# Kernel tuning notes

Measured on AMD Instinct MI355X. Metric: run time of the kernel, lower is better.

Reference implementation:

```python
import jax, jax.numpy as jnp
import numpy as np

B, T, D, H = 2, 4096, 512, 8
DH = D // H  # dim_head = 64


def setup_inputs() -> dict:
    key = jax.random.key(0)
    ks = jax.random.split(key, 10)
    s = 1.0 / np.sqrt(D)
    x = jax.random.normal(ks[0], (B, T, D), dtype=jnp.float32)
    Wq = jax.random.uniform(ks[1], (D, D), jnp.float32, -s, s)
    Wk = jax.random.uniform(ks[2], (D, D), jnp.float32, -s, s)
    Wv = jax.random.uniform(ks[3], (D, D), jnp.float32, -s, s)
    Wo = jax.random.uniform(ks[4], (D, D), jnp.float32, -s, s)
    bq = jnp.zeros((D,), jnp.float32)
    bk = jnp.zeros((D,), jnp.float32)
    bv = jnp.zeros((D,), jnp.float32)
    bo = jnp.zeros((D,), jnp.float32)
    mask = jax.random.randint(ks[5], (1, 1, T, T), 0, 2).astype(bool)
    return {"x": x, "Wq": Wq, "bq": bq, "Wk": Wk, "bk": bk,
            "Wv": Wv, "bv": bv, "Wo": Wo, "bo": bo, "mask": mask}


def reference(x, Wq, bq, Wk, bk, Wv, bv, Wo, bo, mask):
    # QKV projections (self-attention: Q=K=V=x)
    def split_heads(t):
        return t.reshape(B, T, H, DH).transpose(0, 2, 1, 3)  # (B,H,T,DH)
    Q = split_heads(x @ Wq + bq)
    K = split_heads(x @ Wk + bk)
    V = split_heads(x @ Wv + bv)
    # scaled dot-product attention with additive mask penalty (as in source)
    scores = jnp.einsum('bhqd,bhkd->bhqk', Q, K) / np.sqrt(DH)
    scores = scores + (~mask).astype(scores.dtype) * (-1e9)
    att_w = jax.nn.softmax(scores, axis=-1)
    O = jnp.einsum('bhqk,bhkd->bhqd', att_w, V)
    O = O.transpose(0, 2, 1, 3).reshape(B, T, D)
    return O @ Wo + bo
```

## Files before the change

kernel.cpp:

```cpp
#include <hip/hip_runtime.h>
#include <stdint.h>

#define B_ 2
#define T_ 4096
#define D_ 512
#define H_ 8
#define DH_ 64

typedef __bf16 bf16;
typedef __bf16 bf16x4_t __attribute__((ext_vector_type(4)));
typedef __bf16 bf16x8_t __attribute__((ext_vector_type(8)));
typedef float f32x4 __attribute__((ext_vector_type(4)));
typedef short short4_t __attribute__((ext_vector_type(4)));
typedef uint32_t u32;

static constexpr float QSCALE = 0.18033688011112042f;

__device__ __forceinline__ void async16(void* lds, const void* g) {
  __builtin_amdgcn_global_load_lds(
      (const __attribute__((address_space(1))) void*)g,
      (__attribute__((address_space(3))) void*)lds, 16, 0, 0);
}

__global__ __launch_bounds__(256) void prep_kernel(
    const float* __restrict__ x,
    const float* __restrict__ Wq, const float* __restrict__ Wk,
    const float* __restrict__ Wv, const float* __restrict__ Wo,
    const void* __restrict__ maskp,
    bf16* __restrict__ xb, bf16* __restrict__ WTall, bf16* __restrict__ WoT,
    u32* __restrict__ bmask)
{
  int bid = blockIdx.x;
  int tid = threadIdx.x;
  if (bid < 4096) {
    int idx = bid * 256 + tid;
    const float4* xf = (const float4*)x;
    float4 v = xf[idx];
    bf16x4_t o;
    o[0] = (bf16)v.x; o[1] = (bf16)v.y; o[2] = (bf16)v.z; o[3] = (bf16)v.w;
    ((bf16x4_t*)xb)[idx] = o;
  } else if (bid < 8192) {
    int gid = (bid - 4096) * 256 + tid;
    int sel = gid >> 18;
    int idx = gid & 262143;
    int n = idx >> 9, k = idx & 511;
    if (sel < 3) {
      const float* W = (sel == 0) ? Wq : (sel == 1) ? Wk : Wv;
      float v = W[k * 512 + n];
      if (sel == 0) v *= QSCALE;
      WTall[gid] = (bf16)v;
    } else {
      WoT[idx] = (bf16)Wo[k * 512 + n];
    }
  } else {
    int wid = (bid - 8192) * 256 + tid;
    const uint8_t* m8 = (const uint8_t*)maskp;
    bool u8mode = (__ballot(m8[4 * (tid & 63) + 1] != 0) != 0ull);
    int row = wid >> 7, wcol = wid & 127;
    size_t off = (size_t)row * 4096 + (size_t)wcol * 32;
    u32 w = 0;
    if (u8mode) {
      const uint4* p = (const uint4*)(m8 + off);
      uint4 a = p[0], b = p[1];
      u32 ws[8] = {a.x, a.y, a.z, a.w, b.x, b.y, b.z, b.w};
      #pragma unroll
      for (int j = 0; j < 32; ++j)
        if ((ws[j >> 2] >> ((j & 3) * 8)) & 0xffu) w |= (1u << j);
    } else {
      const uint4* p = (const uint4*)((const u32*)maskp + off);
      #pragma unroll
      for (int q = 0; q < 8; ++q) {
        uint4 a = p[q];
        if (a.x) w |= 1u << (q * 4 + 0);
        if (a.y) w |= 1u << (q * 4 + 1);
        if (a.z) w |= 1u << (q * 4 + 2);
        if (a.w) w |= 1u << (q * 4 + 3);
      }
    }
    bmask[((size_t)(row >> 6) * 64 + (wcol >> 1)) * 128 + (row & 63) * 2 + (wcol & 1)] = w;
  }
}

__global__ __launch_bounds__(256) void qkv_kernel(
    const bf16* __restrict__ xb, const bf16* __restrict__ WTall,
    const float* __restrict__ bq, const float* __restrict__ bk,
    const float* __restrict__ bv,
    bf16* __restrict__ Qb, bf16* __restrict__ Kb, bf16* __restrict__ Vtb)
{
  __shared__ char smem[16384];
  char* smX = smem;
  char* smW = smem + 8192;
  int tid = threadIdx.x;
  int lane = tid & 63, wave = tid >> 6;
  int lo = lane & 15, quad = lane >> 4;
  int wr = wave >> 1, wc = wave & 1;
  int bm = blockIdx.x * 64;
  int bn = blockIdx.y * 64;
  int sel = bn >> 9;
  f32x4 acc[2][2] = {};
  for (int kc = 0; kc < 8; ++kc) {
    __syncthreads();
    for (int s = tid; s < 512; s += 256) {
      int row = s >> 3, slot = s & 7;
      int cg = slot ^ (row & 7) ^ ((row >> 3) & 1);
      async16(smX + s * 16, xb + (size_t)(bm + row) * 512 + kc * 64 + cg * 8);
      async16(smW + s * 16, WTall + (size_t)(bn + row) * 512 + kc * 64 + cg * 8);
    }
    __syncthreads();
    #pragma unroll
    for (int ks = 0; ks < 2; ++ks) {
      bf16x8_t a[2], b[2];
      #pragma unroll
      for (int mt = 0; mt < 2; ++mt) {
        int row = wr * 32 + mt * 16 + lo;
        int ch = (ks * 4 + quad) ^ (row & 7) ^ ((row >> 3) & 1);
        a[mt] = *(const bf16x8_t*)(smX + row * 128 + ch * 16);
      }
      #pragma unroll
      for (int nt = 0; nt < 2; ++nt) {
        int row = wc * 32 + nt * 16 + lo;
        int ch = (ks * 4 + quad) ^ (row & 7) ^ ((row >> 3) & 1);
        b[nt] = *(const bf16x8_t*)(smW + row * 128 + ch * 16);
      }
      if (sel < 2) {
        #pragma unroll
        for (int mt = 0; mt < 2; ++mt)
          #pragma unroll
          for (int nt = 0; nt < 2; ++nt)
            acc[mt][nt] = __builtin_amdgcn_mfma_f32_16x16x32_bf16(
                b[nt], a[mt], acc[mt][nt], 0, 0, 0);
      } else {
        #pragma unroll
        for (int mt = 0; mt < 2; ++mt)
          #pragma unroll
          for (int nt = 0; nt < 2; ++nt)
            acc[mt][nt] = __builtin_amdgcn_mfma_f32_16x16x32_bf16(
                a[mt], b[nt], acc[mt][nt], 0, 0, 0);
      }
    }
  }
  int b_ = bm >> 12;
  if (sel < 2) {
    const float* bias = (sel == 0) ? bq : bk;
    bf16* base = (sel == 0) ? Qb : Kb;
    #pragma unroll
    for (int mt = 0; mt < 2; ++mt) {
      int t = (bm & 4095) + wr * 32 + mt * 16 + lo;
      #pragma unroll
      for (int nt = 0; nt < 2; ++nt) {
        int n0 = (bn + wc * 32 + nt * 16 + quad * 4) & 511;
        int h = n0 >> 6, dh0 = n0 & 63;
        bf16x4_t v;
        #pragma unroll
        for (int r = 0; r < 4; ++r) {
          float bs = bias[n0 + r];
          if (sel == 0) bs *= QSCALE;
          v[r] = (bf16)(acc[mt][nt][r] + bs);
        }
        *(bf16x4_t*)(base + (size_t)(b_ * H_ + h) * T_ * DH_ +
                     (size_t)t * 64 + dh0) = v;
      }
    }
  } else {
    #pragma unroll
    for (int nt = 0; nt < 2; ++nt) {
      int n0 = (bn + wc * 32 + nt * 16 + lo) & 511;
      int h = n0 >> 6, dh = n0 & 63;
      float bs = bv[n0];
      #pragma unroll
      for (int mt = 0; mt < 2; ++mt) {
        int t0 = (bm & 4095) + wr * 32 + mt * 16 + quad * 4;
        bf16x4_t v;
        #pragma unroll
        for (int r = 0; r < 4; ++r) v[r] = (bf16)(acc[mt][nt][r] + bs);
        *(bf16x4_t*)(Vtb + ((size_t)(b_ * H_ + h) * DH_ + dh) * T_ + t0) = v;
      }
    }
  }
}

__global__ __launch_bounds__(256, 4) void attn_kernel(
    const bf16* __restrict__ Qb, const bf16* __restrict__ Kb,
    const bf16* __restrict__ Vtb, const u32* __restrict__ bm2,
    bf16* __restrict__ Obuf)
{
  __shared__ char smem[17408];
  char* smK = smem;
  char* smV = smem + 8192;
  u32* smM = (u32*)(smem + 16384);
  float* smL = (float*)(smem + 16896);
  int tid = threadIdx.x;
  int lane = tid & 63, kh = tid >> 6;
  int lo = lane & 15, quad = lane >> 4;
  int blk = blockIdx.x;
  int bh = blk & 15;
  int qt32 = blk >> 4;
  int qbase = qt32 * 32;

  const bf16* Kg = Kb + (size_t)bh * T_ * DH_;
  const bf16* Vg = Vtb + (size_t)bh * DH_ * T_;
  const u32* mg = bm2 + (size_t)(qt32 >> 1) * 8192 + (qt32 & 1) * 64;

  const bf16* Qg = Qb + ((size_t)bh * T_ + qbase) * DH_;
  bf16x8_t qf[2][2];
  #pragma unroll
  for (int qt = 0; qt < 2; ++qt)
    #pragma unroll
    for (int ks = 0; ks < 2; ++ks)
      qf[qt][ks] = *(const bf16x8_t*)(Qg + (qt * 16 + lo) * 64 + ks * 32 + quad * 8);

  short one = (lo == 0) ? (short)0x3F80 : (short)0;
  short4_t ones = {one, one, one, one};

  f32x4 O[2][4] = {};
  f32x4 Ol[2] = {};

  for (int kc = 0; kc < 64; ++kc) {
    __syncthreads();
    #pragma unroll
    for (int i = 0; i < 2; ++i) {
      int s = tid + i * 256;
      int row = s >> 3, slot = s & 7;
      int cg = slot ^ (row & 7) ^ ((row >> 3) & 1);
      async16(smK + s * 16, Kg + (size_t)(kc * 64 + row) * 64 + cg * 8);
      async16(smV + s * 16, Vg + (size_t)row * T_ + kc * 64 + cg * 8);
    }
    if (tid < 16) async16((char*)smM + tid * 16, mg + kc * 128 + tid * 4);
    __syncthreads();
    f32x4 St[2] = {};
    #pragma unroll
    for (int ks = 0; ks < 2; ++ks) {
      int krow = kh * 16 + lo;
      int ch = (ks * 4 + quad) ^ (krow & 7) ^ ((krow >> 3) & 1);
      bf16x8_t kf = *(const bf16x8_t*)(smK + krow * 128 + ch * 16);
      #pragma unroll
      for (int qt = 0; qt < 2; ++qt)
        St[qt] = __builtin_amdgcn_mfma_f32_16x16x32_bf16(
            kf, qf[qt][ks], St[qt], 0, 0, 0);
    }
    short4_t pf[2];
    #pragma unroll
    for (int qt = 0; qt < 2; ++qt) {
      u32 w = smM[(qt * 16 + lo) * 2 + (kh >> 1)] >> ((kh & 1) * 16 + quad * 4);
      bf16x4_t t;
      #pragma unroll
      for (int r = 0; r < 4; ++r) {
        int mb = ((int)(w << (31 - r))) >> 31;
        u32 pe = __builtin_bit_cast(u32, __builtin_amdgcn_exp2f(St[qt][r]));
        t[r] = (bf16)__builtin_bit_cast(float, pe & (u32)mb);
      }
      pf[qt] = __builtin_bit_cast(short4_t, t);
    }
    #pragma unroll
    for (int qt = 0; qt < 2; ++qt)
      Ol[qt] = __builtin_amdgcn_mfma_f32_16x16x16bf16_1k(
          pf[qt], ones, Ol[qt], 0, 0, 0);
    #pragma unroll
    for (int dt = 0; dt < 4; ++dt) {
      int d = dt * 16 + lo;
      int c = (kh * 2 + (quad >> 1)) ^ (d & 7) ^ ((d >> 3) & 1);
      short4_t vf = *(const short4_t*)(
          smV + d * 128 + c * 16 + ((quad & 1) << 3));
      #pragma unroll
      for (int qt = 0; qt < 2; ++qt)
        O[qt][dt] = __builtin_amdgcn_mfma_f32_16x16x16bf16_1k(
            pf[qt], vf, O[qt][dt], 0, 0, 0);
    }
  }
  __syncthreads();
  float* bufA = (float*)smem;
  float* bufB = (float*)(smem + 8320);
  if (lo == 0) {
    #pragma unroll
    for (int qt = 0; qt < 2; ++qt)
      #pragma unroll
      for (int r = 0; r < 4; ++r)
        smL[kh * 32 + qt * 16 + quad * 4 + r] = Ol[qt][r];
  }
  if (kh & 1) {
    float* buf = (kh == 1) ? bufA : bufB;
    #pragma unroll
    for (int qt = 0; qt < 2; ++qt)
      #pragma unroll
      for (int dt = 0; dt < 4; ++dt)
        #pragma unroll
        for (int r = 0; r < 4; ++r)
          buf[(qt * 16 + quad * 4 + r) * 65 + dt * 16 + lo] = O[qt][dt][r];
  }
  __syncthreads();
  if (!(kh & 1)) {
    float* buf = (kh == 0) ? bufA : bufB;
    #pragma unroll
    for (int qt = 0; qt < 2; ++qt)
      #pragma unroll
      for (int dt = 0; dt < 4; ++dt)
        #pragma unroll
        for (int r = 0; r < 4; ++r)
          O[qt][dt][r] += buf[(qt * 16 + quad * 4 + r) * 65 + dt * 16 + lo];
  }
  __syncthreads();
  if (kh == 2) {
    #pragma unroll
    for (int qt = 0; qt < 2; ++qt)
      #pragma unroll
      for (int dt = 0; dt < 4; ++dt)
        #pragma unroll
        for (int r = 0; r < 4; ++r)
          bufB[(qt * 16 + quad * 4 + r) * 65 + dt * 16 + lo] = O[qt][dt][r];
  }
  __syncthreads();
  if (kh == 0) {
    bf16* Og = Obuf + ((size_t)bh * T_ + qbase) * DH_;
    #pragma unroll
    for (int qt = 0; qt < 2; ++qt) {
      #pragma unroll
      for (int r = 0; r < 4; ++r) {
        int q = qt * 16 + quad * 4 + r;
        float tot = (smL[q] + smL[32 + q]) + (smL[64 + q] + smL[96 + q]);
        float inv = 1.0f / tot;
        #pragma unroll
        for (int dt = 0; dt < 4; ++dt) {
          float o = (O[qt][dt][r] + bufB[q * 65 + dt * 16 + lo]) * inv;
          Og[(size_t)q * 64 + dt * 16 + lo] = (bf16)o;
        }
      }
    }
  }
}

__global__ __launch_bounds__(256) void proj_kernel(
    const bf16* __restrict__ Obuf, const bf16* __restrict__ WoT,
    const float* __restrict__ bo, float* __restrict__ out)
{
  __shared__ char smem[16384];
  char* smA = smem;
  char* smW = smem + 8192;
  int tid = threadIdx.x;
  int lane = tid & 63, wave = tid >> 6;
  int lo = lane & 15, quad = lane >> 4;
  int wr = wave >> 1, wc = wave & 1;
  int bm = blockIdx.x * 64;
  int bn = blockIdx.y * 64;
  int b_ = bm >> 12, trow = bm & 4095;
  f32x4 acc[2][2] = {};
  for (int kc = 0; kc < 8; ++kc) {
    __syncthreads();
    const bf16* Ag = Obuf + ((size_t)(b_ * H_ + kc) * T_ + trow) * DH_;
    for (int s = tid; s < 512; s += 256) {
      int row = s >> 3, slot = s & 7;
      int cg = slot ^ (row & 7) ^ ((row >> 3) & 1);
      async16(smA + s * 16, Ag + row * 64 + cg * 8);
      async16(smW + s * 16, WoT + (size_t)(bn + row) * 512 + kc * 64 + cg * 8);
    }
    __syncthreads();
    #pragma unroll
    for (int ks = 0; ks < 2; ++ks) {
      bf16x8_t a[2], b[2];
      #pragma unroll
      for (int mt = 0; mt < 2; ++mt) {
        int row = wr * 32 + mt * 16 + lo;
        int ch = (ks * 4 + quad) ^ (row & 7) ^ ((row >> 3) & 1);
        a[mt] = *(const bf16x8_t*)(smA + row * 128 + ch * 16);
      }
      #pragma unroll
      for (int nt = 0; nt < 2; ++nt) {
        int row = wc * 32 + nt * 16 + lo;
        int ch = (ks * 4 + quad) ^ (row & 7) ^ ((row >> 3) & 1);
        b[nt] = *(const bf16x8_t*)(smW + row * 128 + ch * 16);
      }
      #pragma unroll
      for (int mt = 0; mt < 2; ++mt)
        #pragma unroll
        for (int nt = 0; nt < 2; ++nt)
          acc[mt][nt] = __builtin_amdgcn_mfma_f32_16x16x32_bf16(
              b[nt], a[mt], acc[mt][nt], 0, 0, 0);
    }
  }
  #pragma unroll
  for (int mt = 0; mt < 2; ++mt) {
    int t = bm + wr * 32 + mt * 16 + lo;
    #pragma unroll
    for (int nt = 0; nt < 2; ++nt) {
      int c0 = bn + wc * 32 + nt * 16 + quad * 4;
      float4 v;
      v.x = acc[mt][nt][0] + bo[c0 + 0];
      v.y = acc[mt][nt][1] + bo[c0 + 1];
      v.z = acc[mt][nt][2] + bo[c0 + 2];
      v.w = acc[mt][nt][3] + bo[c0 + 3];
      *(float4*)(out + (size_t)t * 512 + c0) = v;
    }
  }
}

extern "C" void kernel_launch(void* const* d_in, const int* in_sizes, int n_in,
                              void* d_out, int out_size, void* d_ws, size_t ws_size,
                              hipStream_t stream) {
  const float* x  = (const float*)d_in[0];
  const float* Wq = (const float*)d_in[1];
  const float* bq = (const float*)d_in[2];
  const float* Wk = (const float*)d_in[3];
  const float* bk = (const float*)d_in[4];
  const float* Wv = (const float*)d_in[5];
  const float* bv = (const float*)d_in[6];
  const float* Wo = (const float*)d_in[7];
  const float* bo = (const float*)d_in[8];
  const void* maskp = d_in[9];
  float* out = (float*)d_out;

  char* w = (char*)d_ws;
  bf16* xb    = (bf16*)(w);
  bf16* WTall = (bf16*)(w + 8388608);
  bf16* WoT   = (bf16*)(w + 9961472);
  bf16* Qb    = (bf16*)(w + 10485760);
  bf16* Kb    = (bf16*)(w + 18874368);
  bf16* Vtb   = (bf16*)(w + 27262976);
  bf16* Obuf  = (bf16*)(w + 35651584);
  u32*  bmask = (u32*)(w + 44040192);

  prep_kernel<<<10240, 256, 0, stream>>>(x, Wq, Wk, Wv, Wo, maskp,
                                         xb, WTall, WoT, bmask);
  qkv_kernel<<<dim3(128, 24), 256, 0, stream>>>(xb, WTall, bq, bk, bv,
                                                Qb, Kb, Vtb);
  attn_kernel<<<2048, 256, 0, stream>>>(Qb, Kb, Vtb, bmask, Obuf);
  proj_kernel<<<dim3(128, 8), 256, 0, stream>>>(Obuf, WoT, bo, out);
}
```

Measured before the change: 308.2 us.

## Double attention query tile per block to share K/V staging across two query halves

The attention kernel now runs 512 threads per block covering 64 query rows: two groups of four waves share each staged K/V chunk and mask tile, with each group handling 32 queries. The aim is to halve the global-to-LDS K/V traffic and the number of load passes per query, and to halve the block count. The cross-wave reduction of partial outputs becomes a serial chain over three steps with extra barriers, and the launch bounds request 8 waves per EU, which may constrain registers.

```diff
diff --git a/kernel.cpp b/kernel.cpp
--- a/kernel.cpp
+++ b/kernel.cpp
@@ -179,29 +179,31 @@
   }
 }
 
-__global__ __launch_bounds__(256, 4) void attn_kernel(
+__global__ __launch_bounds__(512, 8) void attn_kernel(
     const bf16* __restrict__ Qb, const bf16* __restrict__ Kb,
     const bf16* __restrict__ Vtb, const u32* __restrict__ bm2,
     bf16* __restrict__ Obuf)
 {
-  __shared__ char smem[17408];
+  __shared__ char smem[17920];
   char* smK = smem;
   char* smV = smem + 8192;
   u32* smM = (u32*)(smem + 16384);
   float* smL = (float*)(smem + 16896);
   int tid = threadIdx.x;
-  int lane = tid & 63, kh = tid >> 6;
+  int lane = tid & 63, wv = tid >> 6;
   int lo = lane & 15, quad = lane >> 4;
+  int qh = wv >> 2;
+  int kh = wv & 3;
   int blk = blockIdx.x;
   int bh = blk & 15;
-  int qt32 = blk >> 4;
-  int qbase = qt32 * 32;
+  int qt64 = blk >> 4;
+  int qbase = qt64 * 64;
 
   const bf16* Kg = Kb + (size_t)bh * T_ * DH_;
   const bf16* Vg = Vtb + (size_t)bh * DH_ * T_;
-  const u32* mg = bm2 + (size_t)(qt32 >> 1) * 8192 + (qt32 & 1) * 64;
-
-  const bf16* Qg = Qb + ((size_t)bh * T_ + qbase) * DH_;
+  const u32* mg = bm2 + (size_t)qt64 * 8192;
+
+  const bf16* Qg = Qb + ((size_t)bh * T_ + qbase + qh * 32) * DH_;
   bf16x8_t qf[2][2];
   #pragma unroll
   for (int qt = 0; qt < 2; ++qt)
@@ -217,15 +219,14 @@
 
   for (int kc = 0; kc < 64; ++kc) {
     __syncthreads();
-    #pragma unroll
-    for (int i = 0; i < 2; ++i) {
-      int s = tid + i * 256;
+    {
+      int s = tid;
       int row = s >> 3, slot = s & 7;
       int cg = slot ^ (row & 7) ^ ((row >> 3) & 1);
       async16(smK + s * 16, Kg + (size_t)(kc * 64 + row) * 64 + cg * 8);
       async16(smV + s * 16, Vg + (size_t)row * T_ + kc * 64 + cg * 8);
     }
-    if (tid < 16) async16((char*)smM + tid * 16, mg + kc * 128 + tid * 4);
+    if (tid < 32) async16((char*)smM + tid * 16, mg + kc * 128 + tid * 4);
     __syncthreads();
     f32x4 St[2] = {};
     #pragma unroll
@@ -241,7 +242,8 @@
     short4_t pf[2];
     #pragma unroll
     for (int qt = 0; qt < 2; ++qt) {
-      u32 w = smM[(qt * 16 + lo) * 2 + (kh >> 1)] >> ((kh & 1) * 16 + quad * 4);
+      u32 w = smM[(qh * 32 + qt * 16 + lo) * 2 + (kh >> 1)]
+                  >> ((kh & 1) * 16 + quad * 4);
       bf16x4_t t;
       #pragma unroll
       for (int r = 0; r < 4; ++r) {
@@ -268,17 +270,15 @@
     }
   }
   __syncthreads();
-  float* bufA = (float*)smem;
-  float* bufB = (float*)(smem + 8320);
+  float* buf = (float*)(smem + qh * 8320);
   if (lo == 0) {
     #pragma unroll
     for (int qt = 0; qt < 2; ++qt)
       #pragma unroll
       for (int r = 0; r < 4; ++r)
-        smL[kh * 32 + qt * 16 + quad * 4 + r] = Ol[qt][r];
-  }
-  if (kh & 1) {
-    float* buf = (kh == 1) ? bufA : bufB;
+        smL[kh * 64 + qh * 32 + qt * 16 + quad * 4 + r] = Ol[qt][r];
+  }
+  if (kh == 3) {
     #pragma unroll
     for (int qt = 0; qt < 2; ++qt)
       #pragma unroll
@@ -288,8 +288,7 @@
           buf[(qt * 16 + quad * 4 + r) * 65 + dt * 16 + lo] = O[qt][dt][r];
   }
   __syncthreads();
-  if (!(kh & 1)) {
-    float* buf = (kh == 0) ? bufA : bufB;
+  if (kh == 2) {
     #pragma unroll
     for (int qt = 0; qt < 2; ++qt)
       #pragma unroll
@@ -306,21 +305,42 @@
       for (int dt = 0; dt < 4; ++dt)
         #pragma unroll
         for (int r = 0; r < 4; ++r)
-          bufB[(qt * 16 + quad * 4 + r) * 65 + dt * 16 + lo] = O[qt][dt][r];
+          buf[(qt * 16 + quad * 4 + r) * 65 + dt * 16 + lo] = O[qt][dt][r];
+  }
+  __syncthreads();
+  if (kh == 1) {
+    #pragma unroll
+    for (int qt = 0; qt < 2; ++qt)
+      #pragma unroll
+      for (int dt = 0; dt < 4; ++dt)
+        #pragma unroll
+        for (int r = 0; r < 4; ++r)
+          O[qt][dt][r] += buf[(qt * 16 + quad * 4 + r) * 65 + dt * 16 + lo];
+  }
+  __syncthreads();
+  if (kh == 1) {
+    #pragma unroll
+    for (int qt = 0; qt < 2; ++qt)
+      #pragma unroll
+      for (int dt = 0; dt < 4; ++dt)
+        #pragma unroll
+        for (int r = 0; r < 4; ++r)
+          buf[(qt * 16 + quad * 4 + r) * 65 + dt * 16 + lo] = O[qt][dt][r];
   }
   __syncthreads();
   if (kh == 0) {
-    bf16* Og = Obuf + ((size_t)bh * T_ + qbase) * DH_;
+    bf16* Og = Obuf + ((size_t)bh * T_ + qbase + qh * 32) * DH_;
     #pragma unroll
     for (int qt = 0; qt < 2; ++qt) {
       #pragma unroll
       for (int r = 0; r < 4; ++r) {
         int q = qt * 16 + quad * 4 + r;
-        float tot = (smL[q] + smL[32 + q]) + (smL[64 + q] + smL[96 + q]);
+        int qq = qh * 32 + q;
+        float tot = (smL[qq] + smL[64 + qq]) + (smL[128 + qq] + smL[192 + qq]);
         float inv = 1.0f / tot;
         #pragma unroll
         for (int dt = 0; dt < 4; ++dt) {
-          float o = (O[qt][dt][r] + bufB[q * 65 + dt * 16 + lo]) * inv;
+          float o = (O[qt][dt][r] + buf[q * 65 + dt * 16 + lo]) * inv;
           Og[(size_t)q * 64 + dt * 16 + lo] = (bf16)o;
         }
       }
@@ -421,6 +441,6 @@
                                          xb, WTall, WoT, bmask);
   qkv_kernel<<<dim3(128, 24), 256, 0, stream>>>(xb, WTall, bq, bk, bv,
                                                 Qb, Kb, Vtb);
-  attn_kernel<<<2048, 256, 0, stream>>>(Qb, Kb, Vtb, bmask, Obuf);
+  attn_kernel<<<1024, 512, 0, stream>>>(Qb, Kb, Vtb, bmask, Obuf);
   proj_kernel<<<dim3(128, 8), 256, 0, stream>>>(Obuf, WoT, bo, out);
 }
```

Result: slower. 695.9 us (+125.8%).
